# Kernel tuning notes

Measured on AMD Instinct MI355X. Metric: run time of the kernel, lower is better.

Reference implementation:

```python
import jax, jax.numpy as jnp
import numpy as np

KERNELS = (4, 4, 8, 8, 8, 16, 16)
HEADS = (4, 4, 8, 8, 8, 16, 16)
PATCH = 2
EPS = 1e-5


def _layer_norm(x, w, b):
    mu = jnp.mean(x, axis=-1, keepdims=True)
    var = jnp.mean(jnp.square(x - mu), axis=-1, keepdims=True)
    return (x - mu) * jax.lax.rsqrt(var + EPS) * w + b


def _sliding_kernel_attention(x, w_qkv, k, heads):
    # x: (B, H, W, C) channels-last. Unfold -> per-window attention over the
    # k*k pixels (token dim = C) -> overlap-add fold (stride 1).
    B, H, W, C = x.shape
    Lh, Lw = H - k + 1, W - k + 1
    scale = (C // heads) ** -0.5
    ih = jnp.arange(Lh)[:, None] + jnp.arange(k)[None, :]   # (Lh, k)
    iw = jnp.arange(Lw)[:, None] + jnp.arange(k)[None, :]   # (Lw, k)
    pat = x[:, ih][:, :, :, iw]                             # (B, Lh, k, Lw, k, C)
    tok = pat.transpose(0, 1, 3, 2, 4, 5).reshape(B, Lh * Lw, k * k, C)
    qkv = jnp.einsum('blnc,dc->blnd', tok, w_qkv)           # (B, L, k*k, 3C)
    q, kk, v = jnp.split(qkv, 3, axis=-1)
    attn = jax.nn.softmax(jnp.einsum('blqc,blkc->blqk', q, kk) * scale, axis=-1)
    o = jnp.einsum('blqk,blkc->blqc', attn, v)              # (B, L, k*k, C)
    o = o.reshape(B, Lh, Lw, k, k, C).transpose(0, 1, 3, 2, 4, 5)  # (B,Lh,k,Lw,k,C)
    # overlap-add fold back to (B, H, W, C); duplicate indices accumulate
    return jnp.zeros_like(x).at[:, ih[:, :, None, None], iw[None, None, :, :], :].add(o)


def _block(x, ln1_w, ln1_b, w_qkv, ln2_w, ln2_b, w1, b1, w2, b2, k, heads):
    x = x + _sliding_kernel_attention(_layer_norm(x, ln1_w, ln1_b), w_qkv, k, heads)
    h = _layer_norm(x, ln2_w, ln2_b)
    h = jax.nn.gelu(h @ w1.T + b1, approximate=False)
    return x + (h @ w2.T + b2)


def _forward(x, patch_w, patch_b, row_emb, col_emb, cls_tok, ln1_w, ln1_b, qkv_w,
             ln2_w, ln2_b, mlp_w1, mlp_b1, mlp_w2, mlp_b2, cls_w, cls_b):
    # patch embed: conv k=stride=PATCH; output laid out channels-last (B, G, G, C)
    h = jax.lax.conv_general_dilated(
        x, patch_w, (PATCH, PATCH), 'VALID',
        dimension_numbers=('NCHW', 'OIHW', 'NHWC')) + patch_b
    B, G, _, C = h.shape
    # 2D positional embedding: row half + col half concatenated on channels
    pos = jnp.concatenate([
        jnp.broadcast_to(row_emb[:, None, :], (G, G, C // 2)),
        jnp.broadcast_to(col_emb[None, :, :], (G, G, C // 2))], axis=-1)
    h = h + pos
    # cls token: one extra row prepended along H (torch cat on dim=2)
    cls = jnp.broadcast_to(cls_tok, (B, 1, G, C))
    h = jnp.concatenate([cls, h], axis=1)                   # (B, G+1, G, C)
    for i in range(7):
        h = _block(h, ln1_w[i], ln1_b[i], qkv_w[i], ln2_w[i], ln2_b[i],
                   mlp_w1[i], mlp_b1[i], mlp_w2[i], mlp_b2[i],
                   KERNELS[i], HEADS[i])
    return h[:, 0, 0, :] @ cls_w.T + cls_b                  # (B, num_classes)


def setup_inputs() -> dict:
    key = jax.random.key(0)
    ks = jax.random.split(key, 8)
    B, C, G, NCLS, NB = 16, 256, 16, 1000, 7
    s = 0.02
    return {
        'x': jax.random.normal(ks[0], (B, 3, 32, 32), jnp.float32),
        'patch_w': jax.random.normal(ks[1], (C, 3, PATCH, PATCH), jnp.float32) * s,
        'patch_b': jnp.zeros((C,), jnp.float32),
        'row_emb': jax.random.normal(ks[2], (G, C // 2), jnp.float32) * s,
        'col_emb': jax.random.normal(ks[3], (G, C // 2), jnp.float32) * s,
        'cls_tok': jnp.zeros((C,), jnp.float32),
        'ln1_w': jnp.ones((NB, C), jnp.float32),
        'ln1_b': jnp.zeros((NB, C), jnp.float32),
        'qkv_w': jax.random.normal(ks[4], (NB, 3 * C, C), jnp.float32) * s,
        'ln2_w': jnp.ones((NB, C), jnp.float32),
        'ln2_b': jnp.zeros((NB, C), jnp.float32),
        'mlp_w1': jax.random.normal(ks[5], (NB, 2 * C, C), jnp.float32) * s,
        'mlp_b1': jnp.zeros((NB, 2 * C), jnp.float32),
        'mlp_w2': jax.random.normal(ks[6], (NB, C, 2 * C), jnp.float32) * s,
        'mlp_b2': jnp.zeros((NB, C), jnp.float32),
        'cls_w': jax.random.normal(ks[7], (NCLS, C), jnp.float32) * s,
        'cls_b': jnp.zeros((NCLS,), jnp.float32),
    }


def reference(x, patch_w, patch_b, row_emb, col_emb, cls_tok, ln1_w, ln1_b, qkv_w,
              ln2_w, ln2_b, mlp_w1, mlp_b1, mlp_w2, mlp_b2, cls_w, cls_b):
    return _forward(x, patch_w, patch_b, row_emb, col_emb, cls_tok, ln1_w, ln1_b,
                    qkv_w, ln2_w, ln2_b, mlp_w1, mlp_b1, mlp_w2, mlp_b2, cls_w, cls_b)
```

## Files before the change

kernel.cpp:

```cpp
#include <hip/hip_runtime.h>
#include <cmath>

#define NPIX 4352
#define C_DIM 256

typedef unsigned short ushort_t;
typedef unsigned int uint_t;
typedef float f32x4 __attribute__((ext_vector_type(4)));
typedef __bf16 bfx8 __attribute__((ext_vector_type(8)));

__device__ __forceinline__ ushort_t f2bf(float f) {
    uint_t u = __float_as_uint(f);
    u = (u + 0x7FFFu + ((u >> 16) & 1u)) >> 16;
    return (ushort_t)u;
}
__device__ __forceinline__ float bf2f(ushort_t b) {
    return __uint_as_float(((uint_t)b) << 16);
}
__device__ __forceinline__ float gelu_f(float v) {
    return 0.5f * v * (1.0f + erff(v * 0.70710678118654752f));
}

__global__ __launch_bounds__(256) void conv3_bf16(
    const float* __restrict__ a, ushort_t* __restrict__ oa, int na,
    const float* __restrict__ b, ushort_t* __restrict__ ob, int nb,
    const float* __restrict__ c, ushort_t* __restrict__ oc, int nc)
{
    int ntot = na + nb + nc;
    for (int i = blockIdx.x * 256 + threadIdx.x; i < ntot; i += gridDim.x * 256) {
        if (i < na)            oa[i] = f2bf(a[i]);
        else if (i < na + nb)  ob[i - na] = f2bf(b[i - na]);
        else                   oc[i - na - nb] = f2bf(c[i - na - nb]);
    }
}

__global__ __launch_bounds__(256) void patch_embed_ln(
    const float* __restrict__ x, const float* __restrict__ pw,
    const float* __restrict__ pb, const float* __restrict__ row_emb,
    const float* __restrict__ col_emb, const float* __restrict__ cls_tok,
    const float* __restrict__ lw, const float* __restrict__ lb,
    float* __restrict__ out, ushort_t* __restrict__ lnout)
{
    __shared__ float red[8];
    int p = blockIdx.x;
    int c = threadIdx.x;
    int b = p / 272;
    int rem = p - b * 272;
    int y = rem >> 4;
    int xw = rem & 15;
    float v;
    if (y == 0) {
        v = cls_tok[c];
    } else {
        int gr = y - 1, gc = xw;
        const float* xb = x + (size_t)b * 3 * 1024;
        const float* wc = pw + (size_t)c * 12;
        float acc = pb[c];
        #pragma unroll
        for (int ci = 0; ci < 3; ci++)
            #pragma unroll
            for (int ph = 0; ph < 2; ph++)
                #pragma unroll
                for (int pq = 0; pq < 2; pq++)
                    acc += xb[ci * 1024 + (2 * gr + ph) * 32 + (2 * gc + pq)]
                         * wc[(ci * 2 + ph) * 2 + pq];
        acc += (c < 128) ? row_emb[gr * 128 + c] : col_emb[gc * 128 + (c - 128)];
        v = acc;
    }
    out[(size_t)p * C_DIM + c] = v;
    float s = v;
    s += __shfl_down(s, 32); s += __shfl_down(s, 16); s += __shfl_down(s, 8);
    s += __shfl_down(s, 4);  s += __shfl_down(s, 2);  s += __shfl_down(s, 1);
    if ((c & 63) == 0) red[c >> 6] = s;
    __syncthreads();
    float mu = (red[0] + red[1] + red[2] + red[3]) * (1.0f / 256.0f);
    float d = v - mu;
    float s2 = d * d;
    s2 += __shfl_down(s2, 32); s2 += __shfl_down(s2, 16); s2 += __shfl_down(s2, 8);
    s2 += __shfl_down(s2, 4);  s2 += __shfl_down(s2, 2);  s2 += __shfl_down(s2, 1);
    if ((c & 63) == 0) red[4 + (c >> 6)] = s2;
    __syncthreads();
    float var = (red[4] + red[5] + red[6] + red[7]) * (1.0f / 256.0f);
    lnout[(size_t)p * C_DIM + c] = f2bf(d * rsqrtf(var + 1e-5f) * lw[c] + lb[c]);
}

__global__ __launch_bounds__(256) void layernorm_k(
    const float* __restrict__ in, const float* __restrict__ w,
    const float* __restrict__ b, ushort_t* __restrict__ out)
{
    __shared__ float red[8];
    int r = blockIdx.x, c = threadIdx.x;
    float v = in[(size_t)r * C_DIM + c];
    float s = v;
    s += __shfl_down(s, 32); s += __shfl_down(s, 16); s += __shfl_down(s, 8);
    s += __shfl_down(s, 4);  s += __shfl_down(s, 2);  s += __shfl_down(s, 1);
    if ((c & 63) == 0) red[c >> 6] = s;
    __syncthreads();
    float mu = (red[0] + red[1] + red[2] + red[3]) * (1.0f / 256.0f);
    float d = v - mu;
    float s2 = d * d;
    s2 += __shfl_down(s2, 32); s2 += __shfl_down(s2, 16); s2 += __shfl_down(s2, 8);
    s2 += __shfl_down(s2, 4);  s2 += __shfl_down(s2, 2);  s2 += __shfl_down(s2, 1);
    if ((c & 63) == 0) red[4 + (c >> 6)] = s2;
    __syncthreads();
    float var = (red[4] + red[5] + red[6] + red[7]) * (1.0f / 256.0f);
    out[(size_t)r * C_DIM + c] = f2bf(d * rsqrtf(var + 1e-5f) * w[c] + b[c]);
}

template <int BM, int BN, int MODE>
__global__ __launch_bounds__(256) void gemm_v2(
    const ushort_t* __restrict__ A, const ushort_t* __restrict__ B,
    const float* __restrict__ bias, const float* __restrict__ res,
    void* __restrict__ outp, ushort_t* __restrict__ vT, int K, int ldo)
{
    constexpr int MI = BM / 32, NJ = BN / 32;
    constexpr int AG = BM * 4, BG = BN * 4;
    constexpr int AU = AG / 256, BU = BG / 256;
    constexpr int HALF = (BM + BN) * 32;
    constexpr int STAGE_E = 2 * HALF;
    constexpr int BOUNCE_E = BM * (BN + 8);
    constexpr int SMEM_E = (STAGE_E > BOUNCE_E) ? STAGE_E : BOUNCE_E;
    __shared__ ushort_t sm[SMEM_E];

    int m0 = blockIdx.x * BM, n0 = blockIdx.y * BN;
    int t = threadIdx.x, lane = t & 63, wv = t >> 6;
    int l15 = lane & 15, lg = lane >> 4;
    int wr = wv >> 1, wc = wv & 1;

    const int nt = K / 32;
    f32x4 acc[MI][NJ] = {};
    uint4 ra[AU], rb[BU];

    #pragma unroll
    for (int u = 0; u < AU; u++) {
        int g = t + u * 256, row = g >> 2, p = g & 3;
        int ps = p ^ ((row >> 1) & 3);
        ra[u] = *(const uint4*)(A + (size_t)(m0 + row) * K + ps * 8);
    }
    #pragma unroll
    for (int u = 0; u < BU; u++) {
        int g = t + u * 256, col = g >> 2, p = g & 3;
        int ps = p ^ ((col >> 1) & 3);
        rb[u] = *(const uint4*)(B + (size_t)(n0 + col) * K + ps * 8);
    }
    #pragma unroll
    for (int u = 0; u < AU; u++) *(uint4*)(sm + (t + u * 256) * 8) = ra[u];
    #pragma unroll
    for (int u = 0; u < BU; u++) *(uint4*)(sm + BM * 32 + (t + u * 256) * 8) = rb[u];
    __syncthreads();

    for (int ks = 0; ks < nt; ks++) {
        int coff = (ks & 1) * HALF, noff = ((ks & 1) ^ 1) * HALF;
        if (ks + 1 < nt) {
            int k1 = (ks + 1) * 32;
            #pragma unroll
            for (int u = 0; u < AU; u++) {
                int g = t + u * 256, row = g >> 2, p = g & 3;
                int ps = p ^ ((row >> 1) & 3);
                ra[u] = *(const uint4*)(A + (size_t)(m0 + row) * K + k1 + ps * 8);
            }
            #pragma unroll
            for (int u = 0; u < BU; u++) {
                int g = t + u * 256, col = g >> 2, p = g & 3;
                int ps = p ^ ((col >> 1) & 3);
                rb[u] = *(const uint4*)(B + (size_t)(n0 + col) * K + k1 + ps * 8);
            }
        }
        bfx8 af[MI], bf[NJ];
        #pragma unroll
        for (int i = 0; i < MI; i++) {
            int row = wr * (BM / 2) + i * 16 + l15;
            af[i] = *(const bfx8*)(sm + coff + row * 32 + ((lg ^ ((row >> 1) & 3)) << 3));
        }
        #pragma unroll
        for (int j = 0; j < NJ; j++) {
            int col = wc * (BN / 2) + j * 16 + l15;
            bf[j] = *(const bfx8*)(sm + coff + BM * 32 + col * 32 + ((lg ^ ((col >> 1) & 3)) << 3));
        }
        #pragma unroll
        for (int i = 0; i < MI; i++)
            #pragma unroll
            for (int j = 0; j < NJ; j++)
                acc[i][j] = __builtin_amdgcn_mfma_f32_16x16x32_bf16(af[i], bf[j], acc[i][j], 0, 0, 0);
        if (ks + 1 < nt) {
            #pragma unroll
            for (int u = 0; u < AU; u++) *(uint4*)(sm + noff + (t + u * 256) * 8) = ra[u];
            #pragma unroll
            for (int u = 0; u < BU; u++) *(uint4*)(sm + noff + BM * 32 + (t + u * 256) * 8) = rb[u];
        }
        __syncthreads();
    }

    if (MODE == 0 && n0 >= 512) {
        #pragma unroll
        for (int i = 0; i < MI; i++) {
            int mb = m0 + wr * (BM / 2) + i * 16 + lg * 4;
            #pragma unroll
            for (int j = 0; j < NJ; j++) {
                int nv = n0 - 512 + wc * (BN / 2) + j * 16 + l15;
                ushort4 pk;
                pk.x = f2bf(acc[i][j][0]); pk.y = f2bf(acc[i][j][1]);
                pk.z = f2bf(acc[i][j][2]); pk.w = f2bf(acc[i][j][3]);
                *(ushort4*)&vT[(size_t)nv * NPIX + mb] = pk;
            }
        }
        return;
    }
    if (MODE == 3) {
        float* o = (float*)outp;
        #pragma unroll
        for (int i = 0; i < MI; i++) {
            #pragma unroll
            for (int j = 0; j < NJ; j++) {
                int col = n0 + wc * (BN / 2) + j * 16 + l15;
                float bz = bias[col];
                #pragma unroll
                for (int r = 0; r < 4; r++) {
                    int row = m0 + wr * (BM / 2) + i * 16 + lg * 4 + r;
                    o[(size_t)row * ldo + col] = acc[i][j][r] + bz + res[(size_t)row * ldo + col];
                }
            }
        }
        return;
    }
    __syncthreads();
    #pragma unroll
    for (int i = 0; i < MI; i++) {
        #pragma unroll
        for (int j = 0; j < NJ; j++) {
            int cl = wc * (BN / 2) + j * 16 + l15;
            float bz = (MODE == 2) ? bias[n0 + cl] : 0.0f;
            #pragma unroll
            for (int r = 0; r < 4; r++) {
                int rl = wr * (BM / 2) + i * 16 + lg * 4 + r;
                float v = acc[i][j][r];
                if (MODE == 2) v = gelu_f(v + bz);
                sm[rl * (BN + 8) + cl] = f2bf(v);
            }
        }
    }
    __syncthreads();
    ushort_t* ob = (ushort_t*)outp;
    #pragma unroll
    for (int e = 0; e < BM * BN; e += 2048) {
        int idx = e + t * 8;
        int rl = idx / BN, cl = idx % BN;
        uint4 v = *(const uint4*)(sm + rl * (BN + 8) + cl);
        *(uint4*)&ob[(size_t)(m0 + rl) * ldo + n0 + cl] = v;
    }
}

__device__ __forceinline__ uint2 ld_u4_align(const uint_t* drow, int e0) {
    int d0 = e0 >> 1;
    if (!(e0 & 1)) return make_uint2(drow[d0], drow[d0 + 1]);
    uint_t a = drow[d0], b = drow[d0 + 1], c = drow[d0 + 2];
    return make_uint2((a >> 16) | (b << 16), (b >> 16) | (c << 16));
}
__device__ __forceinline__ uint4 ld_u8_align(const uint_t* drow, int e0) {
    int d0 = e0 >> 1;
    if (!(e0 & 1)) return make_uint4(drow[d0], drow[d0 + 1], drow[d0 + 2], drow[d0 + 3]);
    uint_t a = drow[d0], b = drow[d0 + 1], c = drow[d0 + 2], d = drow[d0 + 3], e = drow[d0 + 4];
    return make_uint4((a >> 16) | (b << 16), (b >> 16) | (c << 16),
                      (c >> 16) | (d << 16), (d >> 16) | (e << 16));
}

__global__ __launch_bounds__(256) void attn_v4(
    const ushort_t* __restrict__ qk, const ushort_t* __restrict__ vT,
    ushort_t* __restrict__ obuf, int w0, int nW, float scale)
{
    __shared__ ushort_t SH[20992];
    const int Lw = 13, L = 182;
    int t = threadIdx.x, lane = t & 63, wv = t >> 6;
    int l15 = lane & 15, lg = lane >> 4;
    int wloc = wv & 1, chalf = wv >> 1;
    int wrel = blockIdx.x * 2 + wloc;
    if (wrel >= nW) wrel = nW - 1;

    int pbs[2];
    #pragma unroll
    for (int w = 0; w < 2; w++) {
        int wi = blockIdx.x * 2 + w;
        if (wi >= nW) wi = nW - 1;
        wi += w0;
        int b = wi / L, lrem = wi % L;
        pbs[w] = b * 272 + (lrem / Lw) * 16 + (lrem % Lw);
    }

    int qpix = pbs[wloc] + ((l15 >> 2) << 4) + (l15 & 3);
    bfx8 qf[8];
    #pragma unroll
    for (int cs = 0; cs < 8; cs++)
        qf[cs] = *(const bfx8*)(qk + (size_t)qpix * 512 + cs * 32 + lg * 8);

    for (int g = t; g < 32 * 32; g += 256) {
        int row = g >> 5, cg = g & 31;
        int pix = pbs[row >> 4] + (((row & 15) >> 2) << 4) + (row & 3);
        uint4 v = *(const uint4*)(qk + (size_t)pix * 512 + 256 + cg * 8);
        *(uint4*)(SH + row * 256 + ((cg ^ (row & 7)) << 3)) = v;
    }
    for (int g = t; g < 256 * 4; g += 256) {
        int cr = g >> 2, q8 = g & 3;
        int w = q8 >> 1, sub = q8 & 1;
        const uint_t* drow = (const uint_t*)(vT + (size_t)cr * NPIX);
        int pix0 = pbs[w] + (sub << 5);
        uint2 a  = ld_u4_align(drow, pix0);
        uint2 b2 = ld_u4_align(drow, pix0 + 16);
        uint4 v = make_uint4(a.x, a.y, b2.x, b2.y);
        *(uint4*)(SH + 8192 + cr * 40 + q8 * 8) = v;
    }
    __syncthreads();

    f32x4 s0 = {};
    #pragma unroll
    for (int cs = 0; cs < 8; cs++) {
        int krow = (wloc << 4) + l15;
        bfx8 kf = *(const bfx8*)(SH + krow * 256 + ((((cs << 2) + lg) ^ (krow & 7)) << 3));
        s0 = __builtin_amdgcn_mfma_f32_16x16x32_bf16(qf[cs], kf, s0, 0, 0, 0);
    }
    float p4[4], lsum[4];
    #pragma unroll
    for (int r = 0; r < 4; r++) {
        float mx = s0[r];
        mx = fmaxf(mx, __shfl_xor(mx, 1));
        mx = fmaxf(mx, __shfl_xor(mx, 2));
        mx = fmaxf(mx, __shfl_xor(mx, 4));
        mx = fmaxf(mx, __shfl_xor(mx, 8));
        p4[r] = __expf(scale * (s0[r] - mx));
        float ps = p4[r];
        ps += __shfl_xor(ps, 1);
        ps += __shfl_xor(ps, 2);
        ps += __shfl_xor(ps, 4);
        ps += __shfl_xor(ps, 8);
        lsum[r] = ps;
    }
    ushort_t* Pw = SH + 18432 + wv * 640;
    #pragma unroll
    for (int r = 0; r < 4; r++) {
        Pw[(lg * 4 + r) * 40 + (wloc << 4) + l15] = f2bf(p4[r]);
        Pw[(lg * 4 + r) * 40 + ((wloc ^ 1) << 4) + l15] = 0;
    }
    asm volatile("s_waitcnt lgkmcnt(0)" ::: "memory");
    __builtin_amdgcn_sched_barrier(0);
    f32x4 o[8] = {};
    {
        bfx8 pf = *(const bfx8*)(Pw + l15 * 40 + (lg << 3));
        #pragma unroll
        for (int j = 0; j < 8; j++) {
            int c = chalf * 128 + (j << 4) + l15;
            bfx8 vf = *(const bfx8*)(SH + 8192 + c * 40 + (lg << 3));
            o[j] = __builtin_amdgcn_mfma_f32_16x16x32_bf16(pf, vf, o[j], 0, 0, 0);
        }
    }
    asm volatile("s_waitcnt lgkmcnt(0)" ::: "memory");
    __syncthreads();
    float inv[4];
    #pragma unroll
    for (int r = 0; r < 4; r++) inv[r] = 1.0f / lsum[r];
    ushort_t* Ep = SH + wv * 2176;
    #pragma unroll
    for (int j = 0; j < 8; j++)
        #pragma unroll
        for (int r = 0; r < 4; r++)
            Ep[(lg * 4 + r) * 136 + (j << 4) + l15] = f2bf(o[j][r] * inv[r]);
    asm volatile("s_waitcnt lgkmcnt(0)" ::: "memory");
    __builtin_amdgcn_sched_barrier(0);
    size_t gb = ((size_t)wrel * 16) * C_DIM + chalf * 128;
    #pragma unroll
    for (int i = 0; i < 4; i++) {
        int off = i * 512 + lane * 8;
        int row = off >> 7, col = off & 127;
        uint4 v = *(const uint4*)(Ep + row * 136 + col);
        *(uint4*)(obuf + gb + (size_t)row * C_DIM + col) = v;
    }
}

__global__ __launch_bounds__(256) void attn_v3(
    const ushort_t* __restrict__ qk, const ushort_t* __restrict__ vT,
    ushort_t* __restrict__ obuf, int w0, float scale)
{
    __shared__ ushort_t SH[24576];
    const int Lw = 9, L = 90;
    int t = threadIdx.x, lane = t & 63, wv = t >> 6;
    int l15 = lane & 15, lg = lane >> 4;
    int wrel = blockIdx.x;
    int widx = w0 + wrel;
    int b = widx / L, lrem = widx % L;
    int pbase = b * 272 + (lrem / Lw) * 16 + (lrem % Lw);
    int qbase = wv * 16;

    int qtok = qbase + l15;
    int qpix = pbase + ((qtok >> 3) << 4) + (qtok & 7);
    bfx8 qf[8];
    #pragma unroll
    for (int cs = 0; cs < 8; cs++)
        qf[cs] = *(const bfx8*)(qk + (size_t)qpix * 512 + cs * 32 + lg * 8);

    for (int g = t; g < 64 * 16; g += 256) {
        int row = g >> 4, cg = g & 15;
        int pix = pbase + ((row >> 3) << 4) + (row & 7);
        uint4 v = *(const uint4*)(qk + (size_t)pix * 512 + 256 + cg * 8);
        *(uint4*)(SH + row * 128 + ((cg ^ (row & 7)) << 3)) = v;
    }
    for (int g = t; g < 256 * 8; g += 256) {
        int cr = g >> 3, c16 = g & 7;
        const uint_t* drow = (const uint_t*)(vT + (size_t)cr * NPIX);
        uint4 v = ld_u8_align(drow, pbase + (c16 << 4));
        *(uint4*)(SH + 8192 + cr * 64 + ((c16 ^ (cr & 7)) << 3)) = v;
    }
    __syncthreads();

    f32x4 s[4];
    #pragma unroll
    for (int j = 0; j < 4; j++) s[j] = f32x4{0.f, 0.f, 0.f, 0.f};
    #pragma unroll
    for (int cs = 0; cs < 4; cs++) {
        #pragma unroll
        for (int j = 0; j < 4; j++) {
            int krow = (j << 4) + l15;
            bfx8 kf = *(const bfx8*)(SH + krow * 128 + ((((cs << 2) + lg) ^ (krow & 7)) << 3));
            s[j] = __builtin_amdgcn_mfma_f32_16x16x32_bf16(qf[cs], kf, s[j], 0, 0, 0);
        }
    }
    __syncthreads();
    for (int g = t; g < 64 * 16; g += 256) {
        int row = g >> 4, cg = g & 15;
        int pix = pbase + ((row >> 3) << 4) + (row & 7);
        uint4 v = *(const uint4*)(qk + (size_t)pix * 512 + 384 + cg * 8);
        *(uint4*)(SH + row * 128 + ((cg ^ (row & 7)) << 3)) = v;
    }
    __syncthreads();
    #pragma unroll
    for (int cs = 4; cs < 8; cs++) {
        #pragma unroll
        for (int j = 0; j < 4; j++) {
            int krow = (j << 4) + l15;
            bfx8 kf = *(const bfx8*)(SH + krow * 128 + (((((cs - 4) << 2) + lg) ^ (krow & 7)) << 3));
            s[j] = __builtin_amdgcn_mfma_f32_16x16x32_bf16(qf[cs], kf, s[j], 0, 0, 0);
        }
    }
    float p[4][4], lsum[4];
    #pragma unroll
    for (int r = 0; r < 4; r++) {
        float mx = s[0][r];
        #pragma unroll
        for (int j = 1; j < 4; j++) mx = fmaxf(mx, s[j][r]);
        mx = fmaxf(mx, __shfl_xor(mx, 1));
        mx = fmaxf(mx, __shfl_xor(mx, 2));
        mx = fmaxf(mx, __shfl_xor(mx, 4));
        mx = fmaxf(mx, __shfl_xor(mx, 8));
        float ps = 0.f;
        #pragma unroll
        for (int j = 0; j < 4; j++) {
            p[j][r] = __expf(scale * (s[j][r] - mx));
            ps += p[j][r];
        }
        ps += __shfl_xor(ps, 1);
        ps += __shfl_xor(ps, 2);
        ps += __shfl_xor(ps, 4);
        ps += __shfl_xor(ps, 8);
        lsum[r] = ps;
    }
    __syncthreads();
    ushort_t* Pw = SH + wv * 1088;
    #pragma unroll
    for (int j = 0; j < 4; j++)
        #pragma unroll
        for (int r = 0; r < 4; r++)
            Pw[(lg * 4 + r) * 68 + (j << 4) + l15] = f2bf(p[j][r]);
    asm volatile("s_waitcnt lgkmcnt(0)" ::: "memory");
    __builtin_amdgcn_sched_barrier(0);
    f32x4 o[16] = {};
    #pragma unroll
    for (int kt = 0; kt < 2; kt++) {
        bfx8 pf = *(const bfx8*)(Pw + l15 * 68 + (kt << 5) + (lg << 3));
        #pragma unroll
        for (int j = 0; j < 16; j++) {
            int cr = (j << 4) + l15;
            int c16 = ((kt << 2) + lg) ^ (cr & 7);
            bfx8 vf = *(const bfx8*)(SH + 8192 + cr * 64 + (c16 << 3));
            o[j] = __builtin_amdgcn_mfma_f32_16x16x32_bf16(pf, vf, o[j], 0, 0, 0);
        }
    }
    asm volatile("s_waitcnt lgkmcnt(0)" ::: "memory");
    __syncthreads();
    float inv[4];
    #pragma unroll
    for (int r = 0; r < 4; r++) inv[r] = 1.0f / lsum[r];
    ushort_t* Ep = SH + wv * 4224;
    #pragma unroll
    for (int j = 0; j < 16; j++)
        #pragma unroll
        for (int r = 0; r < 4; r++)
            Ep[(lg * 4 + r) * 264 + (j << 4) + l15] = f2bf(o[j][r] * inv[r]);
    asm volatile("s_waitcnt lgkmcnt(0)" ::: "memory");
    __builtin_amdgcn_sched_barrier(0);
    size_t gb = ((size_t)wrel * 64 + qbase) * C_DIM;
    #pragma unroll
    for (int i = 0; i < 8; i++) {
        int off = i * 512 + lane * 8;
        int row = off >> 8, col = off & 255;
        uint4 v = *(const uint4*)(Ep + row * 264 + col);
        *(uint4*)(obuf + gb + off) = v;
    }
}

template <int PASS>
__global__ __launch_bounds__(256) void gemm_seq(
    const ushort_t* __restrict__ A, const ushort_t* __restrict__ B,
    const float* __restrict__ linv, void* __restrict__ outp)
{
    __shared__ ushort_t sm[8192];
    int m0 = blockIdx.x * 64, n0 = blockIdx.y * 64;
    int seq = blockIdx.z;
    int pbase = (seq >> 1) * 272 + (seq & 1) * 16;
    int t = threadIdx.x, lane = t & 63, wv = t >> 6;
    int l15 = lane & 15, lg = lane >> 4;
    int wr = wv >> 1, wc = wv & 1;

    f32x4 acc[2][2] = {};
    uint4 ra, rb;

    int g_row = t >> 2, g_p = t & 3;
    int g_ps = g_p ^ ((g_row >> 1) & 3);

    const ushort_t* Asrc;
    const ushort_t* Bsrc;
    if (PASS == 0) {
        Asrc = A + (size_t)(pbase + m0 + g_row) * 512 + g_ps * 8;
        Bsrc = B + (size_t)(pbase + n0 + g_row) * 512 + 256 + g_ps * 8;
    } else {
        Asrc = A + (size_t)seq * 65536 + (size_t)(m0 + g_row) * 256 + g_ps * 8;
        Bsrc = B + (size_t)(n0 + g_row) * NPIX + pbase + g_ps * 8;
    }

    ra = *(const uint4*)(Asrc);
    rb = *(const uint4*)(Bsrc);
    *(uint4*)(sm + t * 8) = ra;
    *(uint4*)(sm + 2048 + t * 8) = rb;
    __syncthreads();

    for (int ks = 0; ks < 8; ks++) {
        int coff = (ks & 1) * 4096, noff = ((ks & 1) ^ 1) * 4096;
        if (ks + 1 < 8) {
            int k1 = (ks + 1) * 32;
            ra = *(const uint4*)(Asrc + k1);
            rb = *(const uint4*)(Bsrc + k1);
        }
        bfx8 af[2], bf[2];
        #pragma unroll
        for (int i = 0; i < 2; i++) {
            int row = wr * 32 + i * 16 + l15;
            af[i] = *(const bfx8*)(sm + coff + row * 32 + ((lg ^ ((row >> 1) & 3)) << 3));
        }
        #pragma unroll
        for (int j = 0; j < 2; j++) {
            int col = wc * 32 + j * 16 + l15;
            bf[j] = *(const bfx8*)(sm + coff + 2048 + col * 32 + ((lg ^ ((col >> 1) & 3)) << 3));
        }
        #pragma unroll
        for (int i = 0; i < 2; i++)
            #pragma unroll
            for (int j = 0; j < 2; j++)
                acc[i][j] = __builtin_amdgcn_mfma_f32_16x16x32_bf16(af[i], bf[j], acc[i][j], 0, 0, 0);
        if (ks + 1 < 8) {
            *(uint4*)(sm + noff + t * 8) = ra;
            *(uint4*)(sm + noff + 2048 + t * 8) = rb;
        }
        __syncthreads();
    }

    if (PASS == 0) {
        float* S = (float*)outp + (size_t)seq * 65536;
        #pragma unroll
        for (int i = 0; i < 2; i++) {
            #pragma unroll
            for (int j = 0; j < 2; j++) {
                int col = n0 + wc * 32 + j * 16 + l15;
                #pragma unroll
                for (int r = 0; r < 4; r++) {
                    int row = m0 + wr * 32 + i * 16 + lg * 4 + r;
                    S[(size_t)row * 256 + col] = acc[i][j][r];
                }
            }
        }
        return;
    }
    ushort_t* ob = (ushort_t*)outp;
    #pragma unroll
    for (int i = 0; i < 2; i++) {
        #pragma unroll
        for (int j = 0; j < 2; j++) {
            int cl = wc * 32 + j * 16 + l15;
            #pragma unroll
            for (int r = 0; r < 4; r++) {
                int rl = wr * 32 + i * 16 + lg * 4 + r;
                float v = acc[i][j][r] * linv[seq * 256 + m0 + rl];
                sm[rl * 72 + cl] = f2bf(v);
            }
        }
    }
    __syncthreads();
    #pragma unroll
    for (int e = 0; e < 4096; e += 2048) {
        int idx = e + t * 8;
        int rl = idx >> 6, cl = idx & 63;
        uint4 v = *(const uint4*)(sm + rl * 72 + cl);
        *(uint4*)&ob[(size_t)seq * 65536 + (size_t)(m0 + rl) * 256 + n0 + cl] = v;
    }
}

__global__ __launch_bounds__(256) void rowsm(
    const float* __restrict__ sbuf, ushort_t* __restrict__ pbuf,
    float* __restrict__ linv, float scale)
{
    __shared__ float red[8];
    int r = blockIdx.x, t = threadIdx.x;
    float s = sbuf[(size_t)r * 256 + t];
    float m = s;
    m = fmaxf(m, __shfl_down(m, 32)); m = fmaxf(m, __shfl_down(m, 16));
    m = fmaxf(m, __shfl_down(m, 8));  m = fmaxf(m, __shfl_down(m, 4));
    m = fmaxf(m, __shfl_down(m, 2));  m = fmaxf(m, __shfl_down(m, 1));
    if ((t & 63) == 0) red[t >> 6] = m;
    __syncthreads();
    m = fmaxf(fmaxf(red[0], red[1]), fmaxf(red[2], red[3]));
    float p = __expf(scale * (s - m));
    float ps = p;
    ps += __shfl_down(ps, 32); ps += __shfl_down(ps, 16); ps += __shfl_down(ps, 8);
    ps += __shfl_down(ps, 4);  ps += __shfl_down(ps, 2);  ps += __shfl_down(ps, 1);
    if ((t & 63) == 0) red[4 + (t >> 6)] = ps;
    __syncthreads();
    float sum = red[4] + red[5] + red[6] + red[7];
    pbuf[(size_t)r * 256 + t] = f2bf(p);
    if (t == 0) linv[r] = 1.0f / sum;
}

template <int K>
__global__ __launch_bounds__(256) void foldA(
    const ushort_t* __restrict__ obuf, float* __restrict__ rowsum)
{
    constexpr int Lh = 18 - K, Lw = 17 - K, L = Lh * Lw, T = K * K;
    int c = threadIdx.x;
    int bid = blockIdx.x;
    int dy = bid % K;
    int blh = bid / K;
    int lh = blh % Lh;
    int b = blh / Lh;
    float acc[16];
    #pragma unroll
    for (int x = 0; x < 16; x++) acc[x] = 0.f;
    const ushort_t* base = obuf + ((size_t)(b * L + lh * Lw) * T + dy * K) * C_DIM + c;
    #pragma unroll
    for (int lw = 0; lw < Lw; lw++)
        #pragma unroll
        for (int dx = 0; dx < K; dx++)
            acc[lw + dx] += bf2f(base[((size_t)lw * T + dx) * C_DIM]);
    float* orow = rowsum + (size_t)bid * 16 * C_DIM + c;
    #pragma unroll
    for (int x = 0; x < 16; x++) orow[(size_t)x * C_DIM] = acc[x];
}

template <int K>
__global__ __launch_bounds__(256) void foldB(
    const float* __restrict__ rowsum, const float* __restrict__ xin,
    float* __restrict__ y, const float* __restrict__ lw_,
    const float* __restrict__ lb_, ushort_t* __restrict__ lnout)
{
    constexpr int Lh = 18 - K;
    __shared__ float red[8];
    int p = blockIdx.x, c = threadIdx.x;
    int b = p / 272, rem = p - b * 272;
    int yy = rem >> 4, xx = rem & 15;
    float acc = xin[(size_t)p * C_DIM + c];
    #pragma unroll
    for (int dy = 0; dy < K; dy++) {
        int lh = yy - dy;
        if (lh >= 0 && lh < Lh)
            acc += rowsum[(((size_t)(b * Lh + lh) * K + dy) * 16 + xx) * C_DIM + c];
    }
    y[(size_t)p * C_DIM + c] = acc;
    float s = acc;
    s += __shfl_down(s, 32); s += __shfl_down(s, 16); s += __shfl_down(s, 8);
    s += __shfl_down(s, 4);  s += __shfl_down(s, 2);  s += __shfl_down(s, 1);
    if ((c & 63) == 0) red[c >> 6] = s;
    __syncthreads();
    float mu = (red[0] + red[1] + red[2] + red[3]) * (1.0f / 256.0f);
    float d = acc - mu;
    float s2 = d * d;
    s2 += __shfl_down(s2, 32); s2 += __shfl_down(s2, 16); s2 += __shfl_down(s2, 8);
    s2 += __shfl_down(s2, 4);  s2 += __shfl_down(s2, 2);  s2 += __shfl_down(s2, 1);
    if ((c & 63) == 0) red[4 + (c >> 6)] = s2;
    __syncthreads();
    float var = (red[4] + red[5] + red[6] + red[7]) * (1.0f / 256.0f);
    lnout[(size_t)p * C_DIM + c] = f2bf(d * rsqrtf(var + 1e-5f) * lw_[c] + lb_[c]);
}

__global__ __launch_bounds__(256) void foldB16(
    const ushort_t* __restrict__ obuf, const float* __restrict__ xin,
    float* __restrict__ y, const float* __restrict__ lw_,
    const float* __restrict__ lb_, ushort_t* __restrict__ lnout)
{
    __shared__ float red[8];
    int p = blockIdx.x, c = threadIdx.x;
    int b = p / 272, rem = p - b * 272;
    int yy = rem >> 4, xx = rem & 15;
    float acc = xin[(size_t)p * C_DIM + c];
    if (yy <= 15)
        acc += bf2f(obuf[((size_t)(b * 2) * 256 + (yy * 16 + xx)) * C_DIM + c]);
    if (yy >= 1)
        acc += bf2f(obuf[((size_t)(b * 2 + 1) * 256 + ((yy - 1) * 16 + xx)) * C_DIM + c]);
    y[(size_t)p * C_DIM + c] = acc;
    float s = acc;
    s += __shfl_down(s, 32); s += __shfl_down(s, 16); s += __shfl_down(s, 8);
    s += __shfl_down(s, 4);  s += __shfl_down(s, 2);  s += __shfl_down(s, 1);
    if ((c & 63) == 0) red[c >> 6] = s;
    __syncthreads();
    float mu = (red[0] + red[1] + red[2] + red[3]) * (1.0f / 256.0f);
    float d = acc - mu;
    float s2 = d * d;
    s2 += __shfl_down(s2, 32); s2 += __shfl_down(s2, 16); s2 += __shfl_down(s2, 8);
    s2 += __shfl_down(s2, 4);  s2 += __shfl_down(s2, 2);  s2 += __shfl_down(s2, 1);
    if ((c & 63) == 0) red[4 + (c >> 6)] = s2;
    __syncthreads();
    float var = (red[4] + red[5] + red[6] + red[7]) * (1.0f / 256.0f);
    lnout[(size_t)p * C_DIM + c] = f2bf(d * rsqrtf(var + 1e-5f) * lw_[c] + lb_[c]);
}

__global__ __launch_bounds__(256) void fold_ln(
    const ushort_t* __restrict__ obuf, const float* __restrict__ xin,
    float* __restrict__ y, const float* __restrict__ lw,
    const float* __restrict__ lb, ushort_t* __restrict__ lnout, int do_ln,
    int k, int Lh, int Lw, int w0, int w1)
{
    __shared__ float red[8];
    int p = blockIdx.x;
    int c = threadIdx.x;
    int b = p / 272;
    int rem = p - b * 272;
    int yy = rem >> 4, xx = rem & 15;
    int L = Lh * Lw;
    int T = k * k;
    float acc = xin ? xin[(size_t)p * C_DIM + c] : y[(size_t)p * C_DIM + c];
    int lh0 = max(0, yy - k + 1), lh1 = min(Lh - 1, yy);
    int lw0 = max(0, xx - k + 1), lw1 = min(Lw - 1, xx);
    for (int lh = lh0; lh <= lh1; lh++) {
        for (int lw = lw0; lw <= lw1; lw++) {
            int widx = b * L + lh * Lw + lw;
            if (widx < w0 || widx >= w1) continue;
            int n = (yy - lh) * k + (xx - lw);
            acc += bf2f(obuf[((size_t)(widx - w0) * T + n) * C_DIM + c]);
        }
    }
    y[(size_t)p * C_DIM + c] = acc;
    if (!do_ln) return;
    float s = acc;
    s += __shfl_down(s, 32); s += __shfl_down(s, 16); s += __shfl_down(s, 8);
    s += __shfl_down(s, 4);  s += __shfl_down(s, 2);  s += __shfl_down(s, 1);
    if ((c & 63) == 0) red[c >> 6] = s;
    __syncthreads();
    float mu = (red[0] + red[1] + red[2] + red[3]) * (1.0f / 256.0f);
    float d = acc - mu;
    float s2 = d * d;
    s2 += __shfl_down(s2, 32); s2 += __shfl_down(s2, 16); s2 += __shfl_down(s2, 8);
    s2 += __shfl_down(s2, 4);  s2 += __shfl_down(s2, 2);  s2 += __shfl_down(s2, 1);
    if ((c & 63) == 0) red[4 + (c >> 6)] = s2;
    __syncthreads();
    float var = (red[4] + red[5] + red[6] + red[7]) * (1.0f / 256.0f);
    lnout[(size_t)p * C_DIM + c] = f2bf(d * rsqrtf(var + 1e-5f) * lw[c] + lb[c]);
}

__global__ __launch_bounds__(256) void classifier_k(
    const float* __restrict__ h, const float* __restrict__ cw,
    const float* __restrict__ cb, float* __restrict__ out)
{
    __shared__ float hrow[256];
    int b = blockIdx.x;
    int n = blockIdx.y * 256 + threadIdx.x;
    hrow[threadIdx.x] = h[(size_t)b * 272 * C_DIM + threadIdx.x];
    __syncthreads();
    if (n < 1000) {
        float acc = cb[n];
        const float* wr = cw + (size_t)n * C_DIM;
        for (int c = 0; c < 256; c++) acc += hrow[c] * wr[c];
        out[(size_t)b * 1000 + n] = acc;
    }
}

extern "C" void kernel_launch(void* const* d_in, const int* in_sizes, int n_in,
                              void* d_out, int out_size, void* d_ws, size_t ws_size,
                              hipStream_t stream)
{
    const float* x       = (const float*)d_in[0];
    const float* patch_w = (const float*)d_in[1];
    const float* patch_b = (const float*)d_in[2];
    const float* row_emb = (const float*)d_in[3];
    const float* col_emb = (const float*)d_in[4];
    const float* cls_tok = (const float*)d_in[5];
    const float* ln1_w   = (const float*)d_in[6];
    const float* ln1_b   = (const float*)d_in[7];
    const float* qkv_w   = (const float*)d_in[8];
    const float* ln2_w   = (const float*)d_in[9];
    const float* ln2_b   = (const float*)d_in[10];
    const float* mlp_w1  = (const float*)d_in[11];
    const float* mlp_b1  = (const float*)d_in[12];
    const float* mlp_w2  = (const float*)d_in[13];
    const float* mlp_b2  = (const float*)d_in[14];
    const float* cls_w   = (const float*)d_in[15];
    const float* cls_b   = (const float*)d_in[16];
    float* out = (float*)d_out;

    float* xb0  = (float*)d_ws;
    float* xb1  = xb0 + (size_t)NPIX * 256;
    ushort_t* lnb = (ushort_t*)(xb1 + (size_t)NPIX * 256);
    ushort_t* qkb = lnb + (size_t)NPIX * 256;
    ushort_t* vT  = qkb + (size_t)NPIX * 512;
    ushort_t* h1  = vT + (size_t)256 * NPIX;
    ushort_t* wq  = h1 + (size_t)NPIX * 512;
    ushort_t* w1b = wq + (size_t)7 * 768 * 256;
    ushort_t* w2b = w1b + (size_t)7 * 512 * 256;
    float* scratch = (float*)(w2b + (size_t)7 * 256 * 512);
    float* rowsum  = scratch;
    float* sbuf    = scratch;
    ushort_t* pbuf = (ushort_t*)(sbuf + (size_t)32 * 65536);
    float* linv    = (float*)(pbuf + (size_t)32 * 65536);
    ushort_t* obuf = (ushort_t*)(rowsum + 5242880);
    size_t obuf_off_bytes = (size_t)((char*)obuf - (char*)d_ws);
    size_t obuf_cap_e = (ws_size > obuf_off_bytes + 64)
                        ? (ws_size - obuf_off_bytes - 64) / 2 : 0;

    conv3_bf16<<<1024, 256, 0, stream>>>(qkv_w, wq, 7 * 768 * 256,
                                         mlp_w1, w1b, 7 * 512 * 256,
                                         mlp_w2, w2b, 7 * 256 * 512);

    patch_embed_ln<<<NPIX, 256, 0, stream>>>(x, patch_w, patch_b, row_emb,
                                             col_emb, cls_tok, ln1_w, ln1_b,
                                             xb0, lnb);

    const int KS[7] = {4, 4, 8, 8, 8, 16, 16};
    float* xcur = xb0;
    float* ybuf = xb1;

    for (int i = 0; i < 7; i++) {
        int k = KS[i];
        int Lh = 18 - k, Lw = 17 - k, L = Lh * Lw, T = k * k;
        float scale = 1.0f / std::sqrt((float)(256 / k));

        if (i > 0)
            layernorm_k<<<NPIX, 256, 0, stream>>>(xcur, ln1_w + i * 256,
                                                  ln1_b + i * 256, lnb);
        gemm_v2<128, 128, 0><<<dim3(NPIX / 128, 6), 256, 0, stream>>>(
            lnb, wq + (size_t)i * 768 * 256, nullptr, nullptr, qkb, vT, 256, 512);

        int totalW = 16 * L;
        if (k == 16) {
            gemm_seq<0><<<dim3(4, 4, 32), 256, 0, stream>>>(qkb, qkb, nullptr, sbuf);
            rowsm<<<8192, 256, 0, stream>>>(sbuf, pbuf, linv, scale);
            gemm_seq<1><<<dim3(4, 4, 32), 256, 0, stream>>>(pbuf, vT, linv, obuf);
            foldB16<<<NPIX, 256, 0, stream>>>(obuf, xcur, ybuf,
                                              ln2_w + i * 256, ln2_b + i * 256, lnb);
        } else if ((size_t)totalW * T * C_DIM <= obuf_cap_e) {
            if (k == 4) {
                attn_v4<<<(totalW + 1) / 2, 256, 0, stream>>>(qkb, vT, obuf, 0, totalW, scale);
                foldA<4><<<16 * 14 * 4, 256, 0, stream>>>(obuf, rowsum);
                foldB<4><<<NPIX, 256, 0, stream>>>(rowsum, xcur, ybuf,
                                                   ln2_w + i * 256, ln2_b + i * 256, lnb);
            } else {
                attn_v3<<<totalW, 256, 0, stream>>>(qkb, vT, obuf, 0, scale);
                foldA<8><<<16 * 10 * 8, 256, 0, stream>>>(obuf, rowsum);
                foldB<8><<<NPIX, 256, 0, stream>>>(rowsum, xcur, ybuf,
                                                   ln2_w + i * 256, ln2_b + i * 256, lnb);
            }
        } else {
            size_t perW = (size_t)T * C_DIM;
            int maxW = (int)(obuf_cap_e / perW);
            if (maxW < 2) maxW = 2;
            if (k == 4) maxW &= ~1;
            for (int w0 = 0; w0 < totalW; w0 += maxW) {
                int nW = totalW - w0 < maxW ? totalW - w0 : maxW;
                if (k == 4)
                    attn_v4<<<(nW + 1) / 2, 256, 0, stream>>>(qkb, vT, obuf, w0, nW, scale);
                else
                    attn_v3<<<nW, 256, 0, stream>>>(qkb, vT, obuf, w0, scale);
                int last = (w0 + nW >= totalW);
                fold_ln<<<NPIX, 256, 0, stream>>>(obuf, (w0 == 0) ? xcur : nullptr,
                                                  ybuf, ln2_w + i * 256, ln2_b + i * 256,
                                                  lnb, last, k, Lh, Lw, w0, w0 + nW);
            }
        }

        gemm_v2<64, 128, 2><<<dim3(NPIX / 64, 4), 256, 0, stream>>>(
            lnb, w1b + (size_t)i * 512 * 256, mlp_b1 + i * 512, nullptr, h1, nullptr, 256, 512);
        gemm_v2<64, 64, 3><<<dim3(NPIX / 64, 4), 256, 0, stream>>>(
            h1, w2b + (size_t)i * 256 * 512, mlp_b2 + i * 256, ybuf, xcur, nullptr, 512, 256);
    }

    classifier_k<<<dim3(16, 4), 256, 0, stream>>>(xcur, cls_w, cls_b, out);
}
```

Measured before the change: 633.4 us.

## Fuse k=8 window attention with horizontal overlap-add into strip kernel

Replaces the per-window k=8 attention kernel, which wrote each window's full output to a global buffer, plus the separate foldA reduction, with a strip kernel. Each block walks the 9 horizontal window positions of one window row, handles half of the channels, and accumulates the overlap-add in an fp32 shared-memory row accumulator before writing row sums directly. This removes the large intermediate obuf round trip and one kernel launch. In exchange there is much less block-level parallelism (320 blocks, each looping serially), large shared-memory use that limits occupancy, and K is recomputed for each channel half.

```diff
diff --git a/kernel.cpp b/kernel.cpp
--- a/kernel.cpp
+++ b/kernel.cpp
@@ -374,133 +374,140 @@
     }
 }
 
-__global__ __launch_bounds__(256) void attn_v3(
+__global__ __launch_bounds__(256) void attn_strip8(
     const ushort_t* __restrict__ qk, const ushort_t* __restrict__ vT,
-    ushort_t* __restrict__ obuf, int w0, float scale)
-{
-    __shared__ ushort_t SH[24576];
-    const int Lw = 9, L = 90;
+    float* __restrict__ rowsum, float scale)
+{
+    __shared__ ushort_t SH[20736 + 32768];
+    float* RA = (float*)(SH + 20736);
+    const int Lh = 10, Lw = 9;
+
     int t = threadIdx.x, lane = t & 63, wv = t >> 6;
     int l15 = lane & 15, lg = lane >> 4;
-    int wrel = blockIdx.x;
-    int widx = w0 + wrel;
-    int b = widx / L, lrem = widx % L;
-    int pbase = b * 272 + (lrem / Lw) * 16 + (lrem % Lw);
-    int qbase = wv * 16;
-
-    int qtok = qbase + l15;
-    int qpix = pbase + ((qtok >> 3) << 4) + (qtok & 7);
+    int bid = blockIdx.x;
+    int ch = bid & 1, slh = bid >> 1;
+    int lh = slh % Lh, b = slh / Lh;
+    int pbase = b * 272 + lh * 16;
+
+    for (int i = t; i < 4096; i += 256)
+        *(f32x4*)(RA + i * 4) = f32x4{0.f, 0.f, 0.f, 0.f};
+
     bfx8 qf[8];
-    #pragma unroll
-    for (int cs = 0; cs < 8; cs++)
-        qf[cs] = *(const bfx8*)(qk + (size_t)qpix * 512 + cs * 32 + lg * 8);
-
-    for (int g = t; g < 64 * 16; g += 256) {
-        int row = g >> 4, cg = g & 15;
-        int pix = pbase + ((row >> 3) << 4) + (row & 7);
-        uint4 v = *(const uint4*)(qk + (size_t)pix * 512 + 256 + cg * 8);
-        *(uint4*)(SH + row * 128 + ((cg ^ (row & 7)) << 3)) = v;
-    }
-    for (int g = t; g < 256 * 8; g += 256) {
-        int cr = g >> 3, c16 = g & 7;
-        const uint_t* drow = (const uint_t*)(vT + (size_t)cr * NPIX);
-        uint4 v = ld_u8_align(drow, pbase + (c16 << 4));
-        *(uint4*)(SH + 8192 + cr * 64 + ((c16 ^ (cr & 7)) << 3)) = v;
-    }
-    __syncthreads();
-
-    f32x4 s[4];
-    #pragma unroll
-    for (int j = 0; j < 4; j++) s[j] = f32x4{0.f, 0.f, 0.f, 0.f};
-    #pragma unroll
-    for (int cs = 0; cs < 4; cs++) {
-        #pragma unroll
-        for (int j = 0; j < 4; j++) {
-            int krow = (j << 4) + l15;
-            bfx8 kf = *(const bfx8*)(SH + krow * 128 + ((((cs << 2) + lg) ^ (krow & 7)) << 3));
-            s[j] = __builtin_amdgcn_mfma_f32_16x16x32_bf16(qf[cs], kf, s[j], 0, 0, 0);
-        }
-    }
-    __syncthreads();
-    for (int g = t; g < 64 * 16; g += 256) {
-        int row = g >> 4, cg = g & 15;
-        int pix = pbase + ((row >> 3) << 4) + (row & 7);
-        uint4 v = *(const uint4*)(qk + (size_t)pix * 512 + 384 + cg * 8);
-        *(uint4*)(SH + row * 128 + ((cg ^ (row & 7)) << 3)) = v;
-    }
-    __syncthreads();
-    #pragma unroll
-    for (int cs = 4; cs < 8; cs++) {
-        #pragma unroll
-        for (int j = 0; j < 4; j++) {
-            int krow = (j << 4) + l15;
-            bfx8 kf = *(const bfx8*)(SH + krow * 128 + (((((cs - 4) << 2) + lg) ^ (krow & 7)) << 3));
-            s[j] = __builtin_amdgcn_mfma_f32_16x16x32_bf16(qf[cs], kf, s[j], 0, 0, 0);
-        }
-    }
-    float p[4][4], lsum[4];
-    #pragma unroll
-    for (int r = 0; r < 4; r++) {
-        float mx = s[0][r];
-        #pragma unroll
-        for (int j = 1; j < 4; j++) mx = fmaxf(mx, s[j][r]);
-        mx = fmaxf(mx, __shfl_xor(mx, 1));
-        mx = fmaxf(mx, __shfl_xor(mx, 2));
-        mx = fmaxf(mx, __shfl_xor(mx, 4));
-        mx = fmaxf(mx, __shfl_xor(mx, 8));
-        float ps = 0.f;
-        #pragma unroll
-        for (int j = 0; j < 4; j++) {
-            p[j][r] = __expf(scale * (s[j][r] - mx));
-            ps += p[j][r];
-        }
-        ps += __shfl_xor(ps, 1);
-        ps += __shfl_xor(ps, 2);
-        ps += __shfl_xor(ps, 4);
-        ps += __shfl_xor(ps, 8);
-        lsum[r] = ps;
-    }
-    __syncthreads();
-    ushort_t* Pw = SH + wv * 1088;
-    #pragma unroll
-    for (int j = 0; j < 4; j++)
-        #pragma unroll
-        for (int r = 0; r < 4; r++)
-            Pw[(lg * 4 + r) * 68 + (j << 4) + l15] = f2bf(p[j][r]);
-    asm volatile("s_waitcnt lgkmcnt(0)" ::: "memory");
-    __builtin_amdgcn_sched_barrier(0);
-    f32x4 o[16] = {};
-    #pragma unroll
-    for (int kt = 0; kt < 2; kt++) {
-        bfx8 pf = *(const bfx8*)(Pw + l15 * 68 + (kt << 5) + (lg << 3));
-        #pragma unroll
-        for (int j = 0; j < 16; j++) {
-            int cr = (j << 4) + l15;
-            int c16 = ((kt << 2) + lg) ^ (cr & 7);
-            bfx8 vf = *(const bfx8*)(SH + 8192 + cr * 64 + (c16 << 3));
-            o[j] = __builtin_amdgcn_mfma_f32_16x16x32_bf16(pf, vf, o[j], 0, 0, 0);
-        }
-    }
-    asm volatile("s_waitcnt lgkmcnt(0)" ::: "memory");
-    __syncthreads();
-    float inv[4];
-    #pragma unroll
-    for (int r = 0; r < 4; r++) inv[r] = 1.0f / lsum[r];
-    ushort_t* Ep = SH + wv * 4224;
-    #pragma unroll
-    for (int j = 0; j < 16; j++)
-        #pragma unroll
-        for (int r = 0; r < 4; r++)
-            Ep[(lg * 4 + r) * 264 + (j << 4) + l15] = f2bf(o[j][r] * inv[r]);
-    asm volatile("s_waitcnt lgkmcnt(0)" ::: "memory");
-    __builtin_amdgcn_sched_barrier(0);
-    size_t gb = ((size_t)wrel * 64 + qbase) * C_DIM;
-    #pragma unroll
-    for (int i = 0; i < 8; i++) {
-        int off = i * 512 + lane * 8;
-        int row = off >> 8, col = off & 255;
-        uint4 v = *(const uint4*)(Ep + row * 264 + col);
-        *(uint4*)(obuf + gb + off) = v;
+    {
+        int qtok = wv * 16 + l15;
+        int qpix = pbase + ((qtok >> 3) << 4) + (qtok & 7);
+        #pragma unroll
+        for (int cs = 0; cs < 8; cs++)
+            qf[cs] = *(const bfx8*)(qk + (size_t)qpix * 512 + cs * 32 + lg * 8);
+    }
+    ushort_t* Pw = SH + 16384 + wv * 1088;
+
+    for (int lw = 0; lw < Lw; lw++) {
+        __syncthreads();
+        for (int g = t; g < 1024; g += 256) {
+            int row = g >> 4, cg = g & 15;
+            int pix = pbase + ((row >> 3) << 4) + lw + (row & 7);
+            uint4 v = *(const uint4*)(qk + (size_t)pix * 512 + 256 + cg * 8);
+            *(uint4*)(SH + row * 128 + ((cg ^ (row & 7)) << 3)) = v;
+        }
+        for (int g = t; g < 1024; g += 256) {
+            int cr = g >> 3, c16 = g & 7;
+            const uint_t* drow = (const uint_t*)(vT + (size_t)(ch * 128 + cr) * NPIX);
+            uint4 v = ld_u8_align(drow, pbase + (c16 << 4) + lw);
+            *(uint4*)(SH + 8192 + cr * 64 + ((c16 ^ (cr & 7)) << 3)) = v;
+        }
+        __syncthreads();
+        f32x4 s[4] = {};
+        #pragma unroll
+        for (int cs = 0; cs < 4; cs++)
+            #pragma unroll
+            for (int j = 0; j < 4; j++) {
+                int krow = (j << 4) + l15;
+                bfx8 kf = *(const bfx8*)(SH + krow * 128 + ((((cs << 2) + lg) ^ (krow & 7)) << 3));
+                s[j] = __builtin_amdgcn_mfma_f32_16x16x32_bf16(qf[cs], kf, s[j], 0, 0, 0);
+            }
+        __syncthreads();
+        for (int g = t; g < 1024; g += 256) {
+            int row = g >> 4, cg = g & 15;
+            int pix = pbase + ((row >> 3) << 4) + lw + (row & 7);
+            uint4 v = *(const uint4*)(qk + (size_t)pix * 512 + 384 + cg * 8);
+            *(uint4*)(SH + row * 128 + ((cg ^ (row & 7)) << 3)) = v;
+        }
+        __syncthreads();
+        #pragma unroll
+        for (int cs = 4; cs < 8; cs++)
+            #pragma unroll
+            for (int j = 0; j < 4; j++) {
+                int krow = (j << 4) + l15;
+                bfx8 kf = *(const bfx8*)(SH + krow * 128 + (((((cs - 4) << 2) + lg) ^ (krow & 7)) << 3));
+                s[j] = __builtin_amdgcn_mfma_f32_16x16x32_bf16(qf[cs], kf, s[j], 0, 0, 0);
+            }
+        if (lw + 1 < Lw) {
+            int qtok = wv * 16 + l15;
+            int qpix = pbase + ((qtok >> 3) << 4) + (lw + 1) + (qtok & 7);
+            #pragma unroll
+            for (int cs = 0; cs < 8; cs++)
+                qf[cs] = *(const bfx8*)(qk + (size_t)qpix * 512 + cs * 32 + lg * 8);
+        }
+        float p[4][4], lsum[4];
+        #pragma unroll
+        for (int r = 0; r < 4; r++) {
+            float mx = s[0][r];
+            #pragma unroll
+            for (int j = 1; j < 4; j++) mx = fmaxf(mx, s[j][r]);
+            mx = fmaxf(mx, __shfl_xor(mx, 1));
+            mx = fmaxf(mx, __shfl_xor(mx, 2));
+            mx = fmaxf(mx, __shfl_xor(mx, 4));
+            mx = fmaxf(mx, __shfl_xor(mx, 8));
+            float ps = 0.f;
+            #pragma unroll
+            for (int j = 0; j < 4; j++) {
+                p[j][r] = __expf(scale * (s[j][r] - mx));
+                ps += p[j][r];
+            }
+            ps += __shfl_xor(ps, 1);
+            ps += __shfl_xor(ps, 2);
+            ps += __shfl_xor(ps, 4);
+            ps += __shfl_xor(ps, 8);
+            lsum[r] = ps;
+        }
+        #pragma unroll
+        for (int j = 0; j < 4; j++)
+            #pragma unroll
+            for (int r = 0; r < 4; r++)
+                Pw[(lg * 4 + r) * 68 + (j << 4) + l15] = f2bf(p[j][r]);
+        asm volatile("s_waitcnt lgkmcnt(0)" ::: "memory");
+        __builtin_amdgcn_sched_barrier(0);
+        f32x4 o[8] = {};
+        #pragma unroll
+        for (int kt = 0; kt < 2; kt++) {
+            bfx8 pf = *(const bfx8*)(Pw + l15 * 68 + (kt << 5) + (lg << 3));
+            #pragma unroll
+            for (int j = 0; j < 8; j++) {
+                int cr = (j << 4) + l15;
+                bfx8 vf = *(const bfx8*)(SH + 8192 + cr * 64 + ((((kt << 2) + lg) ^ (cr & 7)) << 3));
+                o[j] = __builtin_amdgcn_mfma_f32_16x16x32_bf16(pf, vf, o[j], 0, 0, 0);
+            }
+        }
+        float inv[4];
+        #pragma unroll
+        for (int r = 0; r < 4; r++) inv[r] = 1.0f / lsum[r];
+        int dy = wv * 2 + (lg >> 1);
+        int xb = lw + ((lg & 1) << 2);
+        #pragma unroll
+        for (int r = 0; r < 4; r++) {
+            int rab = (dy * 16 + xb + r) * 128;
+            #pragma unroll
+            for (int j = 0; j < 8; j++)
+                RA[rab + (j << 4) + l15] += o[j][r] * inv[r];
+        }
+    }
+    __syncthreads();
+    for (int i = t; i < 4096; i += 256) {
+        f32x4 v = *(const f32x4*)(RA + i * 4);
+        int a = i * 4;
+        int row2 = a >> 7, cl = a & 127;
+        *(f32x4*)(rowsum + (size_t)slh * 32768 + row2 * 256 + ch * 128 + cl) = v;
     }
 }
 
@@ -850,40 +857,36 @@
         gemm_v2<128, 128, 0><<<dim3(NPIX / 128, 6), 256, 0, stream>>>(
             lnb, wq + (size_t)i * 768 * 256, nullptr, nullptr, qkb, vT, 256, 512);
 
-        int totalW = 16 * L;
         if (k == 16) {
             gemm_seq<0><<<dim3(4, 4, 32), 256, 0, stream>>>(qkb, qkb, nullptr, sbuf);
             rowsm<<<8192, 256, 0, stream>>>(sbuf, pbuf, linv, scale);
             gemm_seq<1><<<dim3(4, 4, 32), 256, 0, stream>>>(pbuf, vT, linv, obuf);
             foldB16<<<NPIX, 256, 0, stream>>>(obuf, xcur, ybuf,
                                               ln2_w + i * 256, ln2_b + i * 256, lnb);
-        } else if ((size_t)totalW * T * C_DIM <= obuf_cap_e) {
-            if (k == 4) {
+        } else if (k == 8) {
+            attn_strip8<<<16 * 10 * 2, 256, 0, stream>>>(qkb, vT, rowsum, scale);
+            foldB<8><<<NPIX, 256, 0, stream>>>(rowsum, xcur, ybuf,
+                                               ln2_w + i * 256, ln2_b + i * 256, lnb);
+        } else {
+            int totalW = 16 * L;
+            if ((size_t)totalW * T * C_DIM <= obuf_cap_e) {
                 attn_v4<<<(totalW + 1) / 2, 256, 0, stream>>>(qkb, vT, obuf, 0, totalW, scale);
                 foldA<4><<<16 * 14 * 4, 256, 0, stream>>>(obuf, rowsum);
                 foldB<4><<<NPIX, 256, 0, stream>>>(rowsum, xcur, ybuf,
                                                    ln2_w + i * 256, ln2_b + i * 256, lnb);
             } else {
-                attn_v3<<<totalW, 256, 0, stream>>>(qkb, vT, obuf, 0, scale);
-                foldA<8><<<16 * 10 * 8, 256, 0, stream>>>(obuf, rowsum);
-                foldB<8><<<NPIX, 256, 0, stream>>>(rowsum, xcur, ybuf,
-                                                   ln2_w + i * 256, ln2_b + i * 256, lnb);
-            }
-        } else {
-            size_t perW = (size_t)T * C_DIM;
-            int maxW = (int)(obuf_cap_e / perW);
-            if (maxW < 2) maxW = 2;
-            if (k == 4) maxW &= ~1;
-            for (int w0 = 0; w0 < totalW; w0 += maxW) {
-                int nW = totalW - w0 < maxW ? totalW - w0 : maxW;
-                if (k == 4)
+                size_t perW = (size_t)T * C_DIM;
+                int maxW = (int)(obuf_cap_e / perW);
+                if (maxW < 2) maxW = 2;
+                maxW &= ~1;
+                for (int w0 = 0; w0 < totalW; w0 += maxW) {
+                    int nW = totalW - w0 < maxW ? totalW - w0 : maxW;
                     attn_v4<<<(nW + 1) / 2, 256, 0, stream>>>(qkb, vT, obuf, w0, nW, scale);
-                else
-                    attn_v3<<<nW, 256, 0, stream>>>(qkb, vT, obuf, w0, scale);
-                int last = (w0 + nW >= totalW);
-                fold_ln<<<NPIX, 256, 0, stream>>>(obuf, (w0 == 0) ? xcur : nullptr,
-                                                  ybuf, ln2_w + i * 256, ln2_b + i * 256,
-                                                  lnb, last, k, Lh, Lw, w0, w0 + nW);
+                    int last = (w0 + nW >= totalW);
+                    fold_ln<<<NPIX, 256, 0, stream>>>(obuf, (w0 == 0) ? xcur : nullptr,
+                                                      ybuf, ln2_w + i * 256, ln2_b + i * 256,
+                                                      lnb, last, k, Lh, Lw, w0, w0 + nW);
+                }
             }
         }
 
```

Result: slower. 803.6 us (+26.9%).
